# Kernel optimization log

Hardware: AMD Instinct MI355X
Metric: run time of the kernel (lower is better)

The kernel has to match this reference:

```python
import jax, jax.numpy as jnp
import numpy as np

B, D, L, H, W, T = 256, 512, 32, 14, 14, 8


def _lin(x, w, b=None):
    y = x @ w.T
    return y if b is None else y + b


def _conv1x1(x, w, b):  # x: [B,C,H,W], w: [O,C], b: [O]
    return jnp.einsum('oc,bchw->bohw', w, x) + b[None, :, None, None]


def setup_inputs() -> dict:
    key = jax.random.key(0)
    ks = jax.random.split(key, 24)
    s = 0.02
    inp = {
        'c': jax.random.normal(ks[0], (B, D), jnp.float32),
        'm': jax.random.normal(ks[1], (B, D), jnp.float32),
        'k': jax.random.normal(ks[2], (B, D, H, W), jnp.float32),
        'q': jax.random.normal(ks[3], (B, D), jnp.float32),
        'cw': jax.random.normal(ks[4], (B, L, D), jnp.float32),
        'mask': jax.random.randint(ks[5], (B, L), 0, 2, jnp.int32),
        'cs': jax.random.normal(ks[6], (T, B, D), jnp.float32),
        'ms': jax.random.normal(ks[7], (T, B, D), jnp.float32),
        # ControlUnit params
        'Wcq': jax.random.normal(ks[8], (D, 2 * D), jnp.float32) * s,
        'bcq': jnp.zeros((D,), jnp.float32),
        'Wca': jax.random.normal(ks[9], (1, D), jnp.float32) * s,
        'bca': jnp.zeros((1,), jnp.float32),
        # ReadUnit params
        'Wm_r': jax.random.normal(ks[10], (D, D), jnp.float32) * s,
        'bm_r': jnp.zeros((D,), jnp.float32),
        'Wk': jax.random.normal(ks[11], (D, D), jnp.float32) * s,
        'bk': jnp.zeros((D,), jnp.float32),
        'WI': jax.random.normal(ks[12], (D, 2 * D), jnp.float32) * s,
        'bI': jnp.zeros((D,), jnp.float32),
        'Wra': jax.random.normal(ks[13], (D, D), jnp.float32) * s,
        'bra': jnp.zeros((D,), jnp.float32),
        # WriteUnit params
        'Wm_w': jax.random.normal(ks[14], (D, 2 * D), jnp.float32) * s,
        'bm_w': jnp.zeros((D,), jnp.float32),
        'Wsa': jax.random.normal(ks[15], (1, D), jnp.float32) * s,
        'bsa': jnp.zeros((1,), jnp.float32),
        'Wm2': jax.random.normal(ks[16], (D, D), jnp.float32) * s,
        'bm2': jnp.zeros((D,), jnp.float32),
        'Wc': jax.random.normal(ks[17], (1, D), jnp.float32) * s,
        'bc': jnp.ones((1,), jnp.float32),  # linear_c.bias.data.fill_(1)
        'Ws': jax.random.normal(ks[18], (D, D), jnp.float32) * s,
    }
    return inp


def reference(c, m, k, q, cw, mask, cs, ms,
              Wcq, bcq, Wca, bca,
              Wm_r, bm_r, Wk, bk, WI, bI, Wra, bra,
              Wm_w, bm_w, Wsa, bsa, Wm2, bm2, Wc, bc, Ws):
    # ---- ControlUnit ----
    cq = _lin(jnp.concatenate([c, q], axis=1), Wcq, bcq)          # [B,D]
    ca = _lin(cq[:, None, :] * cw, Wca, bca)                      # [B,L,1]
    ca = jnp.where(mask[:, :, None] > 0, ca, -jnp.inf)            # mask padding
    cv = jax.nn.softmax(ca, axis=1)                               # [B,L,1]
    c_new = jnp.sum(cv * cw, axis=1)                              # [B,D]

    # ---- ReadUnit ----
    mI = _lin(m, Wm_r, bm_r)                                      # [B,D]
    I = mI[:, :, None, None] * _conv1x1(k, Wk, bk)                # [B,D,H,W]
    I_ = _conv1x1(jnp.concatenate([I, k], axis=1), WI, bI)        # [B,D,H,W]
    ra = _conv1x1(I_ * c_new[:, :, None, None], Wra, bra)         # [B,D,H,W]
    rv = jax.nn.softmax(ra, axis=1)                               # Softmax2d = over channels
    r = jnp.sum(rv * k, axis=(-1, -2))                            # [B,D]

    # ---- WriteUnit ----
    m_prev = _lin(jnp.concatenate([r, m], axis=1), Wm_w, bm_w)    # [B,D]
    m_ = _lin(m_prev, Wm2, bm2)                                   # [B,D]
    gate = jax.nn.sigmoid(_lin(c_new, Wc, bc))                    # [B,1]
    sa = jax.nn.softmax(_lin(cs * gate[None, :, :], Wsa, bsa), axis=0)  # [T,B,1]
    m_sa = jnp.sum(sa * ms, axis=0)                               # [B,D]
    m_ = m_ + m_sa @ Ws.T
    m_new = gate * m + (1.0 - gate) * m_                          # [B,D]

    return (c_new, m_new, cv, rv)
```

## Files before the change

kernel.cpp:

```cpp
#include <hip/hip_runtime.h>
#include <hip/hip_bf16.h>

#define BB 256
#define DD 512
#define LL 32
#define HWN 196
#define TT 8
#define STEPB 12544

typedef __hip_bfloat16 bf16;
typedef __attribute__((ext_vector_type(8))) short short8;
typedef __attribute__((ext_vector_type(4))) float f32x4;

__device__ __forceinline__ float b2f(bf16 x) { return __bfloat162float(x); }
__device__ __forceinline__ unsigned short f2bu(float x) {
    bf16 h = __float2bfloat16(x);
    return *(unsigned short*)&h;
}
__device__ __forceinline__ float bu2f(unsigned short u) {
    bf16 h = *(bf16*)&u;
    return __bfloat162float(h);
}
#define NEG_INF (-__builtin_huge_valf())

__device__ __forceinline__ void gload_lds16(const void* g, void* l) {
    __builtin_amdgcn_global_load_lds(
        (const __attribute__((address_space(1))) void*)g,
        (__attribute__((address_space(3))) void*)l, 16, 0, 0);
}
__device__ __forceinline__ void gload_lds4(const void* g, void* l) {
    __builtin_amdgcn_global_load_lds(
        (const __attribute__((address_space(1))) void*)g,
        (__attribute__((address_space(3))) void*)l, 4, 0, 0);
}

__global__ __launch_bounds__(256) void cvt3_kernel(
    const float* __restrict__ s0, unsigned short* __restrict__ d0,
    const float* __restrict__ s1, unsigned short* __restrict__ d1,
    const float* __restrict__ s2, unsigned short* __restrict__ d2)
{
    int blk = blockIdx.x, tid = threadIdx.x;
    const float* s; unsigned short* d; int i;
    if (blk < 256)      { s = s0; d = d0; i = blk*256 + tid; }
    else if (blk < 768) { s = s1; d = d1; i = (blk-256)*256 + tid; }
    else                { s = s2; d = d2; i = (blk-768)*256 + tid; }
    float4 f = ((const float4*)s)[i];
    ushort4 u;
    u.x = f2bu(f.x); u.y = f2bu(f.y); u.z = f2bu(f.z); u.w = f2bu(f.w);
    ((ushort4*)d)[i] = u;
}

__global__ __launch_bounds__(256) void pack_x_kernel(
    const float* __restrict__ X, char* __restrict__ Xp)
{
    int b = blockIdx.x, s = blockIdx.y;
    char* chunk = Xp + ((size_t)(b*16 + s))*STEPB;
    for (int i = threadIdx.x; i < 4*HWN; i += 256) {
        int n = i >> 2, kqp = i & 3;
        const float* base = X + ((size_t)b*DD + s*32 + kqp*8)*HWN + n;
        uint v[4];
        #pragma unroll
        for (int h = 0; h < 4; ++h) {
            float f0 = base[(size_t)(2*h+0)*HWN], f1 = base[(size_t)(2*h+1)*HWN];
            v[h] = (uint)f2bu(f0) | ((uint)f2bu(f1) << 16);
        }
        *(uint4*)(chunk + n*64 + kqp*16) = make_uint4(v[0], v[1], v[2], v[3]);
    }
}

__global__ __launch_bounds__(256) void small_gemm_kernel(
    const float* __restrict__ A1, int K1,
    const float* __restrict__ A2, int K2,
    const float* __restrict__ Wt, const float* __restrict__ bias,
    float* __restrict__ outf, int Dout)
{
    __shared__ float xs[1024];
    int b = blockIdx.x, tid = threadIdx.x;
    int K = K1 + K2;
    for (int i = tid; i < K; i += 256) {
        xs[i] = (i < K1) ? A1[(size_t)b*K1 + i] : A2[(size_t)b*K2 + (i - K1)];
    }
    __syncthreads();
    int d = blockIdx.y*256 + tid;
    const float4* wrow = (const float4*)(Wt + (size_t)d * K);
    float acc = 0.f;
    for (int j = 0; j < K/4; ++j) {
        float4 w = wrow[j];
        acc += w.x*xs[j*4] + w.y*xs[j*4+1] + w.z*xs[j*4+2] + w.w*xs[j*4+3];
    }
    if (bias) acc += bias[d];
    outf[(size_t)b*Dout + d] = acc;
}

__global__ __launch_bounds__(256) void control_kernel(
    const float* __restrict__ cq, const float* __restrict__ cw,
    const float* __restrict__ Wca, const float* __restrict__ bca,
    const int* __restrict__ mask,
    float* __restrict__ cnew_f, float* __restrict__ cv_out, float* __restrict__ cnew_out)
{
    __shared__ float u[DD];
    __shared__ float cas[LL];
    __shared__ float cvs[LL];
    int b = blockIdx.x, tid = threadIdx.x;
    for (int d = tid; d < DD; d += 256) u[d] = cq[(size_t)b*DD + d] * Wca[d];
    __syncthreads();
    int wave = tid >> 6, lane = tid & 63;
    float bca0 = bca[0];
    for (int lw = 0; lw < 8; ++lw) {
        int l = wave*8 + lw;
        const float4* w4 = (const float4*)(cw + ((size_t)(b*LL + l))*DD + lane*8);
        float4 wa = w4[0], wb = w4[1];
        const float* uu = &u[lane*8];
        float p = wa.x*uu[0] + wa.y*uu[1] + wa.z*uu[2] + wa.w*uu[3]
                + wb.x*uu[4] + wb.y*uu[5] + wb.z*uu[6] + wb.w*uu[7];
        for (int off = 32; off > 0; off >>= 1) p += __shfl_down(p, off);
        if (lane == 0) {
            float v = p + bca0;
            if (mask[b*LL + l] <= 0) v = NEG_INF;
            cas[l] = v;
        }
    }
    __syncthreads();
    if (tid < LL) {
        float mx = NEG_INF;
        for (int j = 0; j < LL; ++j) mx = fmaxf(mx, cas[j]);
        float s = 0.f;
        for (int j = 0; j < LL; ++j) s += __expf(cas[j] - mx);
        float cv = __expf(cas[tid] - mx) / s;
        cvs[tid] = cv;
        cv_out[b*LL + tid] = cv;
    }
    __syncthreads();
    for (int d = tid; d < DD; d += 256) {
        float acc = 0.f;
        for (int l = 0; l < LL; ++l) acc += cvs[l] * cw[((size_t)(b*LL + l))*DD + d];
        cnew_f[(size_t)b*DD + d] = acc;
        cnew_out[(size_t)b*DD + d] = acc;
    }
}

__global__ __launch_bounds__(512, 4) void conv_mfma_kernel(
    const char* __restrict__ X1p, int ns1,
    const char* __restrict__ X2p, int ns2,
    const unsigned short* __restrict__ Wb, int C,
    const float* __restrict__ bias, const float* __restrict__ oscale,
    void* __restrict__ Yout, int packed_out)
{
    __shared__ __align__(16) char Xs[4][13312];
    int b = blockIdx.x, ot = blockIdx.y;
    int tid = threadIdx.x;
    int wave = tid >> 6, lane = tid & 63;
    int wm = wave >> 2, wn = wave & 3;
    int obase = ot*128 + wm*64;
    int t0 = wn*3;
    int ntn = (wn == 3) ? 4 : 3;
    int ln = lane & 15, lq = lane >> 4;
    int nsteps = ns1 + ns2;

    auto STAGE = [&](int s) {
        const char* chunk = (s < ns1) ? X1p + ((size_t)b*ns1 + s)*STEPB
                                      : X2p + ((size_t)b*ns2 + (s - ns1))*STEPB;
        char* lb = Xs[s & 3];
        gload_lds16(chunk + wave*1024 + lane*16, lb + wave*1024);
        if (wave < 5)       gload_lds16(chunk + (wave+8)*1024 + lane*16, lb + (wave+8)*1024);
        else if (wave == 7) gload_lds4 (chunk + 12288 + lane*4, lb + 12288);
    };
    auto ALOAD = [&](int s, short8* a) {
        #pragma unroll
        for (int mt = 0; mt < 4; ++mt)
            a[mt] = *(const short8*)(Wb + (size_t)(obase + mt*16 + ln)*C + s*32 + lq*8);
    };

    f32x4 acc[4][4];
    #pragma unroll
    for (int mt = 0; mt < 4; ++mt)
        #pragma unroll
        for (int nt = 0; nt < 4; ++nt) acc[mt][nt] = (f32x4){0.f, 0.f, 0.f, 0.f};

    short8 a_cur[4], a_nxt[4];

    STAGE(0);
    STAGE(1);
    __builtin_amdgcn_sched_barrier(0);
    ALOAD(0, a_cur);
    __builtin_amdgcn_sched_barrier(0);
    STAGE(2);

    auto BODY = [&](int s, bool doA, bool doX) {
        __builtin_amdgcn_s_barrier();
        if (doA) ALOAD(s + 1, a_nxt);
        __builtin_amdgcn_sched_barrier(0);
        if (doX) STAGE(s + 3);
        __builtin_amdgcn_sched_barrier(0);
        const char* curb = Xs[s & 3];
        #pragma unroll
        for (int nt = 0; nt < 4; ++nt) {
            if (nt < ntn) {
                int n = (t0 + nt)*16 + ln;
                union { uint4 u; short8 s8; } bb;
                bb.u = *(const uint4*)(curb + n*64 + lq*16);
                #pragma unroll
                for (int mt = 0; mt < 4; ++mt)
                    acc[mt][nt] = __builtin_amdgcn_mfma_f32_16x16x32_bf16(a_cur[mt], bb.s8, acc[mt][nt], 0, 0, 0);
            }
        }
        #pragma unroll
        for (int mt = 0; mt < 4; ++mt) a_cur[mt] = a_nxt[mt];
    };

    for (int s = 0; s <= nsteps - 4; ++s) {
        asm volatile("s_waitcnt vmcnt(2)" ::: "memory");
        __builtin_amdgcn_sched_barrier(0);
        BODY(s, true, true);
    }
    {
        asm volatile("s_waitcnt vmcnt(2)" ::: "memory");
        __builtin_amdgcn_sched_barrier(0);
        BODY(nsteps - 3, true, false);
    }
    {
        asm volatile("s_waitcnt vmcnt(0)" ::: "memory");
        __builtin_amdgcn_sched_barrier(0);
        BODY(nsteps - 2, true, false);
    }
    {
        asm volatile("s_waitcnt vmcnt(0)" ::: "memory");
        __builtin_amdgcn_sched_barrier(0);
        BODY(nsteps - 1, false, false);
    }

    if (packed_out) {
        uint2* Yp = (uint2*)Yout;
        #pragma unroll
        for (int mt = 0; mt < 4; ++mt) {
            int o4 = obase + mt*16 + lq*4;
            int st = o4 >> 5, kqo = (o4 & 31) >> 2;
            uint2* chunk = Yp + (size_t)(b*16 + st)*1568;
            float bo[4], os[4];
            #pragma unroll
            for (int rr = 0; rr < 4; ++rr) {
                bo[rr] = bias[o4 + rr];
                os[rr] = oscale ? oscale[(size_t)b*DD + o4 + rr] : 1.f;
            }
            #pragma unroll
            for (int nt = 0; nt < 4; ++nt) {
                int hw = (t0 + nt)*16 + ln;
                if (nt < ntn && hw < HWN) {
                    unsigned short v[4];
                    #pragma unroll
                    for (int rr = 0; rr < 4; ++rr)
                        v[rr] = f2bu((acc[mt][nt][rr] + bo[rr]) * os[rr]);
                    chunk[hw*8 + kqo] =
                        make_uint2((uint)v[0] | ((uint)v[1] << 16),
                                   (uint)v[2] | ((uint)v[3] << 16));
                }
            }
        }
    } else {
        unsigned short* Y = (unsigned short*)Yout;
        #pragma unroll
        for (int mt = 0; mt < 4; ++mt) {
            #pragma unroll
            for (int rr = 0; rr < 4; ++rr) {
                int o = obase + mt*16 + lq*4 + rr;
                float bo = bias[o];
                float os = oscale ? oscale[(size_t)b*DD + o] : 1.f;
                #pragma unroll
                for (int nt = 0; nt < 4; ++nt) {
                    int hw = (t0 + nt)*16 + ln;
                    if (nt < ntn && hw < HWN) {
                        float v = (acc[mt][nt][rr] + bo) * os;
                        Y[((size_t)b*DD + o)*HWN + hw] = f2bu(v);
                    }
                }
            }
        }
    }
}

__global__ __launch_bounds__(512) void softmax_part_kernel(
    const bf16* __restrict__ ra,
    unsigned short* __restrict__ pm_part, float* __restrict__ ps_part,
    float* __restrict__ r_zero)
{
    int b = blockIdx.x, y = blockIdx.y, tid = threadIdx.x;
    if (y == 0) r_zero[(size_t)b*DD + tid] = 0.f;
    int half = tid >> 8, hw = tid & 255;
    if (hw < HWN) {
        int sl = y*2 + half;
        const bf16* base = ra + ((size_t)b*DD + sl*64)*HWN + hw;
        float m = NEG_INF, s = 0.f;
        for (int c = 0; c < 64; ++c) {
            float x = b2f(base[(size_t)c*HWN]);
            float nm = fmaxf(m, x);
            s = s*__expf(m - nm) + __expf(x - nm);
            m = nm;
        }
        unsigned short pmu = f2bu(m);
        float pmf = bu2f(pmu);
        s *= __expf(m - pmf);
        size_t idx = ((size_t)sl*BB + b)*HWN + hw;
        pm_part[idx] = pmu;
        ps_part[idx] = s;
    }
}

__global__ __launch_bounds__(512) void softmax_rv_kernel(
    const bf16* __restrict__ ra, const float* __restrict__ kin,
    const unsigned short* __restrict__ pm_part, const float* __restrict__ ps_part,
    float* __restrict__ rv, float* __restrict__ r)
{
    __shared__ float mxs[98], sis[98];
    int b = blockIdx.x, h = blockIdx.y, tid = threadIdx.x;
    int hwb = h*98;
    if (tid < 98) {
        int hw = hwb + tid;
        float pmv[8], mx = NEG_INF;
        #pragma unroll
        for (int i = 0; i < 8; ++i) {
            pmv[i] = bu2f(pm_part[((size_t)i*BB + b)*HWN + hw]);
            mx = fmaxf(mx, pmv[i]);
        }
        float s = 0.f;
        #pragma unroll
        for (int i = 0; i < 8; ++i)
            s += ps_part[((size_t)i*BB + b)*HWN + hw] * __expf(pmv[i] - mx);
        mxs[tid] = mx; sis[tid] = 1.f/s;
    }
    __syncthreads();
    int wave = tid >> 6, lane = tid & 63;
    for (int ci = 0; ci < 64; ++ci) {
        int c = wave*64 + ci;
        size_t rowbase = ((size_t)b*DD + c)*HWN + hwb;
        float psum = 0.f;
        #pragma unroll
        for (int g = 0; g < 2; ++g) {
            int j = g*64 + lane;
            if (j < 98) {
                float e = __expf(b2f(ra[rowbase + j]) - mxs[j]) * sis[j];
                rv[rowbase + j] = e;
                psum += e * kin[rowbase + j];
            }
        }
        for (int off = 32; off > 0; off >>= 1) psum += __shfl_down(psum, off);
        if (lane == 0) atomicAdd(&r[(size_t)b*DD + c], psum);
    }
}

__global__ __launch_bounds__(256) void samsa_kernel(
    const float* __restrict__ cs, const float* __restrict__ ms,
    const float* __restrict__ Wsa, const float* __restrict__ bsa,
    const float* __restrict__ cnew, const float* __restrict__ Wc, const float* __restrict__ bc,
    float* __restrict__ gate_out, float* __restrict__ msa)
{
    __shared__ float lg[TT];
    __shared__ float sas[TT];
    __shared__ float xw[DD];
    __shared__ float gsh;
    int b = blockIdx.x, tid = threadIdx.x;
    int wave = tid >> 6, lane = tid & 63;
    for (int d = tid; d < DD; d += 256) xw[d] = Wsa[d];
    __syncthreads();
    for (int tw = 0; tw < 2; ++tw) {
        int t = wave + 4*tw;
        const float4* c4 = (const float4*)(cs + ((size_t)t*BB + b)*DD + lane*8);
        float4 ca = c4[0], cb = c4[1];
        const float* ww = &xw[lane*8];
        float p = ca.x*ww[0] + ca.y*ww[1] + ca.z*ww[2] + ca.w*ww[3]
                + cb.x*ww[4] + cb.y*ww[5] + cb.z*ww[6] + cb.w*ww[7];
        for (int off = 32; off > 0; off >>= 1) p += __shfl_down(p, off);
        if (lane == 0) lg[t] = p;
    }
    if (wave == 0) {
        const float4* w4 = (const float4*)(Wc + lane*8);
        const float* x = &cnew[(size_t)b*DD + lane*8];
        float4 wa = w4[0], wb = w4[1];
        float p = wa.x*x[0] + wa.y*x[1] + wa.z*x[2] + wa.w*x[3]
                + wb.x*x[4] + wb.y*x[5] + wb.z*x[6] + wb.w*x[7];
        for (int off = 32; off > 0; off >>= 1) p += __shfl_down(p, off);
        if (lane == 0) {
            float g = 1.f / (1.f + __expf(-(p + bc[0])));
            gsh = g; gate_out[b] = g;
        }
    }
    __syncthreads();
    if (tid < TT) {
        float g = gsh, b0 = bsa[0];
        float mx = NEG_INF;
        for (int j = 0; j < TT; ++j) mx = fmaxf(mx, g*lg[j] + b0);
        float s = 0.f;
        for (int j = 0; j < TT; ++j) s += __expf(g*lg[j] + b0 - mx);
        sas[tid] = __expf(g*lg[tid] + b0 - mx) / s;
    }
    __syncthreads();
    for (int d = tid; d < DD; d += 256) {
        float acc = 0.f;
        for (int t = 0; t < TT; ++t) acc += sas[t] * ms[((size_t)t*BB + b)*DD + d];
        msa[(size_t)b*DD + d] = acc;
    }
}

__global__ __launch_bounds__(256) void write_final_kernel(
    const float* __restrict__ msa, const float* __restrict__ Ws,
    const float* __restrict__ m, const float* __restrict__ gate,
    const float* __restrict__ mund, float* __restrict__ mnew)
{
    __shared__ float xs[DD];
    int b = blockIdx.x, tid = threadIdx.x;
    for (int i = tid; i < DD; i += 256) xs[i] = msa[(size_t)b*DD + i];
    __syncthreads();
    float g = gate[b];
    int d = blockIdx.y*256 + tid;
    const float4* wrow = (const float4*)(Ws + (size_t)d * DD);
    float acc = 0.f;
    for (int j = 0; j < DD/4; ++j) {
        float4 w = wrow[j];
        acc += w.x*xs[j*4] + w.y*xs[j*4+1] + w.z*xs[j*4+2] + w.w*xs[j*4+3];
    }
    size_t idx = (size_t)b*DD + d;
    mnew[idx] = g * m[idx] + (1.f - g) * (mund[idx] + acc);
}

extern "C" void kernel_launch(void* const* d_in, const int* in_sizes, int n_in,
                              void* d_out, int out_size, void* d_ws, size_t ws_size,
                              hipStream_t stream)
{
    (void)in_sizes; (void)n_in; (void)out_size; (void)ws_size;
    const float* c    = (const float*)d_in[0];
    const float* m    = (const float*)d_in[1];
    const float* k    = (const float*)d_in[2];
    const float* q    = (const float*)d_in[3];
    const float* cw   = (const float*)d_in[4];
    const int*   mask = (const int*)  d_in[5];
    const float* cs   = (const float*)d_in[6];
    const float* ms   = (const float*)d_in[7];
    const float* Wcq  = (const float*)d_in[8];
    const float* bcq  = (const float*)d_in[9];
    const float* Wca  = (const float*)d_in[10];
    const float* bca  = (const float*)d_in[11];
    const float* Wm_r = (const float*)d_in[12];
    const float* bm_r = (const float*)d_in[13];
    const float* Wk   = (const float*)d_in[14];
    const float* bk   = (const float*)d_in[15];
    const float* WI   = (const float*)d_in[16];
    const float* bI   = (const float*)d_in[17];
    const float* Wra  = (const float*)d_in[18];
    const float* bra  = (const float*)d_in[19];
    const float* Wm_w = (const float*)d_in[20];
    const float* bm_w = (const float*)d_in[21];
    const float* Wsa  = (const float*)d_in[22];
    const float* bsa  = (const float*)d_in[23];
    const float* Wm2  = (const float*)d_in[24];
    const float* bm2  = (const float*)d_in[25];
    const float* Wc   = (const float*)d_in[26];
    const float* bc   = (const float*)d_in[27];
    const float* Ws   = (const float*)d_in[28];

    float* out_cnew = (float*)d_out;
    float* out_mnew = out_cnew + BB*DD;
    float* out_cv   = out_mnew + BB*DD;
    float* out_rv   = out_cv + BB*LL;

    char* Ip  = (char*)out_rv;
    char* I2p = (char*)out_rv + 51380224;

    char* w = (char*)d_ws;
    float* s0      = (float*)(w + 0);
    float* s1      = (float*)(w + 524288);
    unsigned short* pm_part = (unsigned short*)(w + 1048576);
    float* ps_part = (float*)(w + 2097152);
    unsigned short* Wkb  = (unsigned short*)(w + 2097152);
    unsigned short* WIb  = (unsigned short*)(w + 2621440);
    unsigned short* Wrab = (unsigned short*)(w + 3670016);
    char* kp_ra = (char*)(w + 4194304);
    float* gate_w  = (float*)(w + 55574528);

    float* cq_w   = s0;
    float* r_w    = s0;
    float* cnew_w = s1;
    float* mI_w   = (float*)(w + 1048576);
    float* mund_w = (float*)(w + 1048576);
    float* mprev_w= (float*)(w + 1572864);
    float* msa_w  = (float*)(w + 1572864);
    unsigned short* ra_w = (unsigned short*)kp_ra;

    cvt3_kernel<<<1024, 256, 0, stream>>>(Wk, Wkb, WI, WIb, Wra, Wrab);

    pack_x_kernel<<<dim3(BB, 16), 256, 0, stream>>>(k, kp_ra);

    small_gemm_kernel<<<dim3(BB,2), 256, 0, stream>>>(c, DD, q, DD, Wcq, bcq, cq_w, DD);
    small_gemm_kernel<<<dim3(BB,2), 256, 0, stream>>>(m, DD, nullptr, 0, Wm_r, bm_r, mI_w, DD);
    control_kernel<<<BB, 256, 0, stream>>>(cq_w, cw, Wca, bca, mask, cnew_w, out_cv, out_cnew);

    conv_mfma_kernel<<<dim3(BB, 4), 512, 0, stream>>>(kp_ra, 16, nullptr, 0,  Wkb,  DD,   bk,  mI_w,   Ip,   1);
    conv_mfma_kernel<<<dim3(BB, 4), 512, 0, stream>>>(Ip,    16, kp_ra,  16,  WIb,  2*DD, bI,  cnew_w, I2p,  1);
    conv_mfma_kernel<<<dim3(BB, 4), 512, 0, stream>>>(I2p,   16, nullptr, 0,  Wrab, DD,   bra, nullptr, ra_w, 0);

    softmax_part_kernel<<<dim3(BB, 4), 512, 0, stream>>>((const bf16*)ra_w, pm_part, ps_part, r_w);
    softmax_rv_kernel<<<dim3(BB, 2), 512, 0, stream>>>((const bf16*)ra_w, k, pm_part, ps_part, out_rv, r_w);

    small_gemm_kernel<<<dim3(BB,2), 256, 0, stream>>>(r_w, DD, m, DD, Wm_w, bm_w, mprev_w, DD);
    small_gemm_kernel<<<dim3(BB,2), 256, 0, stream>>>(mprev_w, DD, nullptr, 0, Wm2, bm2, mund_w, DD);
    samsa_kernel<<<BB, 256, 0, stream>>>(cs, ms, Wsa, bsa, cnew_w, Wc, bc, gate_w, msa_w);
    write_final_kernel<<<dim3(BB,2), 256, 0, stream>>>(msa_w, Ws, m, gate_w, mund_w, out_mnew);
}
```

Before: 950.2 us.

## Swizzle packed activation layout and remap conv waves to 32x112 tiles

The packed X layout now XOR-swizzles each 16-byte quarter by (n>>1)&3, in both the pack kernel and the packed conv output, so the B-fragment reads from LDS hit fewer bank conflicts. The conv wave tiling changes from a 4x4 grid (64 outputs by 3-4 n-tiles) to a 4x2 grid (32 outputs by 6-7 n-tiles). This cuts the number of A-fragment global loads per wave and reuses each B read across fewer MFMAs. The 4-byte tail load is replaced by a clamped 16-byte load, and the occupancy hint in launch_bounds is dropped, which may change register allocation.

```diff
diff --git a/kernel.cpp b/kernel.cpp
--- a/kernel.cpp
+++ b/kernel.cpp
@@ -27,11 +27,6 @@
     __builtin_amdgcn_global_load_lds(
         (const __attribute__((address_space(1))) void*)g,
         (__attribute__((address_space(3))) void*)l, 16, 0, 0);
-}
-__device__ __forceinline__ void gload_lds4(const void* g, void* l) {
-    __builtin_amdgcn_global_load_lds(
-        (const __attribute__((address_space(1))) void*)g,
-        (__attribute__((address_space(3))) void*)l, 4, 0, 0);
 }
 
 __global__ __launch_bounds__(256) void cvt3_kernel(
@@ -64,7 +59,8 @@
             float f0 = base[(size_t)(2*h+0)*HWN], f1 = base[(size_t)(2*h+1)*HWN];
             v[h] = (uint)f2bu(f0) | ((uint)f2bu(f1) << 16);
         }
-        *(uint4*)(chunk + n*64 + kqp*16) = make_uint4(v[0], v[1], v[2], v[3]);
+        int q = kqp ^ ((n>>1)&3);
+        *(uint4*)(chunk + n*64 + q*16) = make_uint4(v[0], v[1], v[2], v[3]);
     }
 }
 
@@ -139,7 +135,7 @@
     }
 }
 
-__global__ __launch_bounds__(512, 4) void conv_mfma_kernel(
+__global__ __launch_bounds__(512) void conv_mfma_kernel(
     const char* __restrict__ X1p, int ns1,
     const char* __restrict__ X2p, int ns2,
     const unsigned short* __restrict__ Wb, int C,
@@ -150,10 +146,10 @@
     int b = blockIdx.x, ot = blockIdx.y;
     int tid = threadIdx.x;
     int wave = tid >> 6, lane = tid & 63;
-    int wm = wave >> 2, wn = wave & 3;
-    int obase = ot*128 + wm*64;
-    int t0 = wn*3;
-    int ntn = (wn == 3) ? 4 : 3;
+    int wm = wave >> 1, wn = wave & 1;
+    int obase = ot*128 + wm*32;
+    int n0 = wn*112;
+    int ntn = wn ? 6 : 7;
     int ln = lane & 15, lq = lane >> 4;
     int nsteps = ns1 + ns2;
 
@@ -162,50 +158,51 @@
                                       : X2p + ((size_t)b*ns2 + (s - ns1))*STEPB;
         char* lb = Xs[s & 3];
         gload_lds16(chunk + wave*1024 + lane*16, lb + wave*1024);
-        if (wave < 5)       gload_lds16(chunk + (wave+8)*1024 + lane*16, lb + (wave+8)*1024);
-        else if (wave == 7) gload_lds4 (chunk + 12288 + lane*4, lb + 12288);
+        if (wave < 5) {
+            int off = (wave+8)*1024 + lane*16;
+            const char* src = chunk + (off < STEPB ? off : 0);
+            gload_lds16(src, lb + (wave+8)*1024);
+        }
     };
-    auto ALOAD = [&](int s, short8* a) {
-        #pragma unroll
-        for (int mt = 0; mt < 4; ++mt)
-            a[mt] = *(const short8*)(Wb + (size_t)(obase + mt*16 + ln)*C + s*32 + lq*8);
+    auto ALOAD = [&](int s, short8& a0, short8& a1) {
+        a0 = *(const short8*)(Wb + (size_t)(obase + ln)*C + s*32 + lq*8);
+        a1 = *(const short8*)(Wb + (size_t)(obase + 16 + ln)*C + s*32 + lq*8);
     };
 
-    f32x4 acc[4][4];
+    f32x4 acc[2][7];
     #pragma unroll
-    for (int mt = 0; mt < 4; ++mt)
-        #pragma unroll
-        for (int nt = 0; nt < 4; ++nt) acc[mt][nt] = (f32x4){0.f, 0.f, 0.f, 0.f};
-
-    short8 a_cur[4], a_nxt[4];
+    for (int mt = 0; mt < 2; ++mt)
+        #pragma unroll
+        for (int nt = 0; nt < 7; ++nt) acc[mt][nt] = (f32x4){0.f, 0.f, 0.f, 0.f};
+
+    short8 a0c, a1c, a0n, a1n;
 
     STAGE(0);
     STAGE(1);
     __builtin_amdgcn_sched_barrier(0);
-    ALOAD(0, a_cur);
+    ALOAD(0, a0c, a1c);
     __builtin_amdgcn_sched_barrier(0);
     STAGE(2);
 
     auto BODY = [&](int s, bool doA, bool doX) {
         __builtin_amdgcn_s_barrier();
-        if (doA) ALOAD(s + 1, a_nxt);
+        if (doA) ALOAD(s + 1, a0n, a1n);
         __builtin_amdgcn_sched_barrier(0);
         if (doX) STAGE(s + 3);
         __builtin_amdgcn_sched_barrier(0);
         const char* curb = Xs[s & 3];
         #pragma unroll
-        for (int nt = 0; nt < 4; ++nt) {
+        for (int nt = 0; nt < 7; ++nt) {
             if (nt < ntn) {
-                int n = (t0 + nt)*16 + ln;
+                int n = n0 + nt*16 + ln;
+                int q = lq ^ ((n>>1)&3);
                 union { uint4 u; short8 s8; } bb;
-                bb.u = *(const uint4*)(curb + n*64 + lq*16);
-                #pragma unroll
-                for (int mt = 0; mt < 4; ++mt)
-                    acc[mt][nt] = __builtin_amdgcn_mfma_f32_16x16x32_bf16(a_cur[mt], bb.s8, acc[mt][nt], 0, 0, 0);
+                bb.u = *(const uint4*)(curb + n*64 + q*16);
+                acc[0][nt] = __builtin_amdgcn_mfma_f32_16x16x32_bf16(a0c, bb.s8, acc[0][nt], 0, 0, 0);
+                acc[1][nt] = __builtin_amdgcn_mfma_f32_16x16x32_bf16(a1c, bb.s8, acc[1][nt], 0, 0, 0);
             }
         }
-        #pragma unroll
-        for (int mt = 0; mt < 4; ++mt) a_cur[mt] = a_nxt[mt];
+        a0c = a0n; a1c = a1n;
     };
 
     for (int s = 0; s <= nsteps - 4; ++s) {
@@ -232,9 +229,10 @@
     if (packed_out) {
         uint2* Yp = (uint2*)Yout;
         #pragma unroll
-        for (int mt = 0; mt < 4; ++mt) {
+        for (int mt = 0; mt < 2; ++mt) {
             int o4 = obase + mt*16 + lq*4;
             int st = o4 >> 5, kqo = (o4 & 31) >> 2;
+            int qh = kqo >> 1, rb = kqo & 1;
             uint2* chunk = Yp + (size_t)(b*16 + st)*1568;
             float bo[4], os[4];
             #pragma unroll
@@ -243,14 +241,15 @@
                 os[rr] = oscale ? oscale[(size_t)b*DD + o4 + rr] : 1.f;
             }
             #pragma unroll
-            for (int nt = 0; nt < 4; ++nt) {
-                int hw = (t0 + nt)*16 + ln;
+            for (int nt = 0; nt < 7; ++nt) {
+                int hw = n0 + nt*16 + ln;
                 if (nt < ntn && hw < HWN) {
                     unsigned short v[4];
                     #pragma unroll
                     for (int rr = 0; rr < 4; ++rr)
                         v[rr] = f2bu((acc[mt][nt][rr] + bo[rr]) * os[rr]);
-                    chunk[hw*8 + kqo] =
+                    int qs = qh ^ ((hw>>1)&3);
+                    chunk[hw*8 + qs*2 + rb] =
                         make_uint2((uint)v[0] | ((uint)v[1] << 16),
                                    (uint)v[2] | ((uint)v[3] << 16));
                 }
@@ -259,15 +258,15 @@
     } else {
         unsigned short* Y = (unsigned short*)Yout;
         #pragma unroll
-        for (int mt = 0; mt < 4; ++mt) {
+        for (int mt = 0; mt < 2; ++mt) {
             #pragma unroll
             for (int rr = 0; rr < 4; ++rr) {
                 int o = obase + mt*16 + lq*4 + rr;
                 float bo = bias[o];
                 float os = oscale ? oscale[(size_t)b*DD + o] : 1.f;
                 #pragma unroll
-                for (int nt = 0; nt < 4; ++nt) {
-                    int hw = (t0 + nt)*16 + ln;
+                for (int nt = 0; nt < 7; ++nt) {
+                    int hw = n0 + nt*16 + ln;
                     if (nt < ntn && hw < HWN) {
                         float v = (acc[mt][nt][rr] + bo) * os;
                         Y[((size_t)b*DD + o)*HWN + hw] = f2bu(v);
```

Measured after the change: 783.5 us. -17.5%, faster.
